# Kernel tuning notes

Measured on AMD Instinct MI355X. Metric: run time of the kernel, lower is better.

Reference implementation:

```python
import jax, jax.numpy as jnp
import numpy as np

N_HEAD = 16
BLOCK_SIZE = 2049  # w2 last dim = block_size - 1 = 2048


def setup_inputs() -> dict:
    key = jax.random.key(0)
    ks = jax.random.split(key, 9)
    B, T, C = 2, 2048, 1024
    hd = C // N_HEAD
    M = BLOCK_SIZE - 1
    return {
        "x": jax.random.normal(ks[0], (B, T, C), jnp.float32),
        "w1_w": jax.random.normal(ks[1], (C, C), jnp.float32) * 0.02,
        "w1_b": jax.random.normal(ks[2], (C,), jnp.float32) * 0.02,
        # torch uniform_(a=-0.001, b=0.001)
        "w2": jax.random.uniform(ks[3], (N_HEAD, hd, M), jnp.float32, -0.001, 0.001),
        "b2": jax.random.normal(ks[4], (M,), jnp.float32) * 0.02,
        "value_w": jax.random.normal(ks[5], (C, C), jnp.float32) * 0.02,
        "value_b": jax.random.normal(ks[6], (C,), jnp.float32) * 0.02,
        "proj_w": jax.random.normal(ks[7], (C, C), jnp.float32) * 0.02,
        "proj_b": jax.random.normal(ks[8], (C,), jnp.float32) * 0.02,
    }


def reference(x, w1_w, w1_b, w2, b2, value_w, value_b, proj_w, proj_b):
    B, T, C = x.shape
    H = N_HEAD
    hd = C // H
    M = w2.shape[-1]  # block_size - 1
    # kernel = relu(w1(x)), split heads -> [B, H, T, hd]
    k = jax.nn.relu(x @ w1_w.T + w1_b).reshape(B, T, H, hd).transpose(0, 2, 1, 3)
    # synthesizer scores: [B, H, T, M]
    attn = jnp.einsum('bhtd,hdm->bhtm', k, w2) + b2
    # causal mask = tril(ones(block,block))[:T, :M] == 0 -> -inf
    causal = jnp.tril(jnp.ones((T, M), dtype=bool))
    attn = jnp.where(causal, attn, -jnp.inf)
    # softmax over first T score columns
    attn = jax.nn.softmax(attn[..., :T], axis=-1)  # [B, H, T, T]
    v = (x @ value_w.T + value_b).reshape(B, T, H, hd).transpose(0, 2, 1, 3)
    out = jnp.einsum('bhts,bhsd->bhtd', attn, v)
    out = out.transpose(0, 2, 1, 3).reshape(B, T, C)
    return out @ proj_w.T + proj_b
```

## Files before the change

kernel.cpp:

```cpp
#include <hip/hip_runtime.h>
#include <math.h>
#include <stdint.h>

typedef __bf16 bf16;
typedef __bf16 bf16x8 __attribute__((ext_vector_type(8)));
typedef __bf16 bf16x4 __attribute__((ext_vector_type(4)));
typedef float f32x4 __attribute__((ext_vector_type(4)));
typedef float f32x16 __attribute__((ext_vector_type(16)));
typedef unsigned int u32;

__device__ __forceinline__ int swz(int row, int chunk) {
    return row * 64 + ((chunk ^ (row & 7)) << 3);
}

__device__ __forceinline__ void gld16(void* lds, const void* g) {
    __builtin_amdgcn_global_load_lds(
        (const __attribute__((address_space(1))) u32*)g,
        (__attribute__((address_space(3))) u32*)lds, 16, 0, 0);
}

__device__ __forceinline__ void stage16(bf16* dst, const bf16* src, size_t srcStride,
                                        int w, int l) {
    #pragma unroll
    for (int i = 0; i < 2; ++i) {
        const int br = w * 16 + i * 8;
        const int r = br + (l >> 3);
        const int gs = (l & 7) ^ (r & 7);
        gld16(dst + br * 64, src + (size_t)r * srcStride + gs * 8);
    }
}

__global__ void cast_bf16_k(const float* __restrict__ src, bf16* __restrict__ dst, int n) {
    const int stride = gridDim.x * blockDim.x * 4;
    for (int i = (blockIdx.x * blockDim.x + threadIdx.x) * 4; i < n; i += stride) {
        float4 v = *(const float4*)(src + i);
        bf16x4 o = {(bf16)v.x, (bf16)v.y, (bf16)v.z, (bf16)v.w};
        *(bf16x4*)(dst + i) = o;
    }
}

__global__ void cast3_bf16_k(const float* __restrict__ s0, bf16* __restrict__ d0,
                             const float* __restrict__ s1, bf16* __restrict__ d1,
                             const float* __restrict__ s2, bf16* __restrict__ d2, int n) {
    const int stride = gridDim.x * blockDim.x * 4;
    for (int i = (blockIdx.x * blockDim.x + threadIdx.x) * 4; i < n; i += stride) {
        float4 v0 = *(const float4*)(s0 + i);
        float4 v1 = *(const float4*)(s1 + i);
        float4 v2 = *(const float4*)(s2 + i);
        bf16x4 o0 = {(bf16)v0.x, (bf16)v0.y, (bf16)v0.z, (bf16)v0.w};
        bf16x4 o1 = {(bf16)v1.x, (bf16)v1.y, (bf16)v1.z, (bf16)v1.w};
        bf16x4 o2 = {(bf16)v2.x, (bf16)v2.y, (bf16)v2.z, (bf16)v2.w};
        *(bf16x4*)(d0 + i) = o0;
        *(bf16x4*)(d1 + i) = o1;
        *(bf16x4*)(d2 + i) = o2;
    }
}

__global__ __launch_bounds__(256) void w2_transpose_k(const float* __restrict__ w2,
                                                      bf16* __restrict__ w2t, int M) {
    __shared__ float Tf[64][65];
    const int h = blockIdx.y, m0 = blockIdx.x * 64, t = threadIdx.x;
    {
        const int dr = t >> 4, c4 = (t & 15) * 4;
        #pragma unroll
        for (int it = 0; it < 4; ++it) {
            const int d = dr + it * 16;
            float4 v = *(const float4*)(w2 + ((size_t)h * 64 + d) * M + m0 + c4);
            Tf[d][c4] = v.x; Tf[d][c4 + 1] = v.y; Tf[d][c4 + 2] = v.z; Tf[d][c4 + 3] = v.w;
        }
    }
    __syncthreads();
    const int m = t >> 2;
    #pragma unroll
    for (int it = 0; it < 2; ++it) {
        const int ch = (t & 3) + it * 4;
        bf16x8 o;
        #pragma unroll
        for (int j = 0; j < 8; ++j) o[j] = (bf16)Tf[ch * 8 + j][m];
        *(bf16x8*)(w2t + ((size_t)h * M + m0 + m) * 64 + ch * 8) = o;
    }
}

__global__ __launch_bounds__(256, 2) void gemm_bf16_k(const bf16* __restrict__ A,
                                                   const bf16* __restrict__ Bw,
                                                   const float* __restrict__ bias,
                                                   const float* __restrict__ bias2,
                                                   float* __restrict__ C0,
                                                   bf16* __restrict__ CK,
                                                   bf16* __restrict__ CV,
                                                   int M, int N, int K, int mode, int Ns)
{
    __shared__ __align__(16) bf16 As[2][128 * 64];
    __shared__ __align__(16) bf16 Bs[2][128 * 64];
    const int tid = threadIdx.x;
    const int w = tid >> 6, l = tid & 63;
    const int wr = w >> 1, wc = w & 1;
    const int lc = l & 15, lg = l >> 4;
    const int row0 = blockIdx.y * 128, col0 = blockIdx.x * 128;

    f32x4 acc[4][4] = {};

    const int nk = K >> 6;
    auto issue = [&](int buf, int k0) {
        #pragma unroll
        for (int i = 0; i < 4; ++i) {
            const int br = (w * 4 + i) * 8;
            const int r = br + (l >> 3);
            const int gs = (l & 7) ^ (r & 7);
            gld16(&As[buf][br * 64], A  + (size_t)(row0 + r) * K + k0 + gs * 8);
            gld16(&Bs[buf][br * 64], Bw + (size_t)(col0 + r) * K + k0 + gs * 8);
        }
    };

    issue(0, 0);
    int cur = 0;
    for (int kt = 0; kt < nk; ++kt) {
        if (kt + 1 < nk) {
            issue(cur ^ 1, (kt + 1) << 6);
            asm volatile("s_waitcnt vmcnt(8)" ::: "memory");
        } else {
            asm volatile("s_waitcnt vmcnt(0)" ::: "memory");
        }
        __builtin_amdgcn_s_barrier();
        #pragma unroll
        for (int ks = 0; ks < 2; ++ks) {
            bf16x8 af[4], bfv[4];
            #pragma unroll
            for (int i = 0; i < 4; ++i) {
                af[i]  = *(const bf16x8*)&As[cur][swz(wr * 64 + i * 16 + lc, ks * 4 + lg)];
                bfv[i] = *(const bf16x8*)&Bs[cur][swz(wc * 64 + i * 16 + lc, ks * 4 + lg)];
            }
            #pragma unroll
            for (int mi = 0; mi < 4; ++mi)
                #pragma unroll
                for (int ni = 0; ni < 4; ++ni)
                    acc[mi][ni] = __builtin_amdgcn_mfma_f32_16x16x32_bf16(af[mi], bfv[ni], acc[mi][ni], 0, 0, 0);
        }
        asm volatile("s_waitcnt lgkmcnt(0)" ::: "memory");
        __builtin_amdgcn_s_barrier();
        cur ^= 1;
    }

    #pragma unroll
    for (int ni = 0; ni < 4; ++ni) {
        const int col = col0 + wc * 64 + ni * 16 + lc;
        #pragma unroll
        for (int mi = 0; mi < 4; ++mi) {
            const int rowb = row0 + wr * 64 + mi * 16 + lg * 4;
            f32x4 v = acc[mi][ni];
            if (mode == 0) {
                const float bv = bias[col];
                #pragma unroll
                for (int r = 0; r < 4; ++r)
                    C0[(size_t)(rowb + r) * N + col] = v[r] + bv;
            } else if (col < Ns) {
                const float bv = bias[col];
                #pragma unroll
                for (int r = 0; r < 4; ++r)
                    CK[(size_t)(rowb + r) * Ns + col] = (bf16)fmaxf(v[r] + bv, 0.f);
            } else {
                const float bv = bias2[col - Ns];
                const int b = rowb >> 11, tt = rowb & 2047;
                bf16x4 o = {(bf16)(v[0] + bv), (bf16)(v[1] + bv),
                            (bf16)(v[2] + bv), (bf16)(v[3] + bv)};
                *(bf16x4*)(CV + ((size_t)b * Ns + (col - Ns)) * 2048 + tt) = o;
            }
        }
    }
}

__global__ __launch_bounds__(256, 2) void synth_attn_v10(const bf16* __restrict__ Kb,
                                                         const bf16* __restrict__ VT,
                                                         const bf16* __restrict__ w2t,
                                                         const float* __restrict__ b2,
                                                         bf16* __restrict__ Ob)
{
    constexpr int T = 2048, C = 1024, M = 2048;
    __shared__ __align__(16) bf16 Wl[3][64 * 64];
    __shared__ __align__(16) bf16 Vl[3][64 * 64];
    __shared__ float b2l[M];
    const int tid = threadIdx.x;
    const int w = tid >> 6, l = tid & 63;
    const int c = l & 31, hi = l >> 5;

    const int bx = blockIdx.x;
    const int hseg = bx >> 8, idx = bx & 255;
    const int jj = idx & 15;
    const int a = hseg ? (15 - jj) : jj;
    const int bh = (hseg << 4) | (idx >> 4);
    const int h = bh & 15, b = bh >> 4;
    const int tA = a, tB = 31 - a;
    const int myT = (w >> 1) ? tA : tB;
    const int t0w = myT * 64 + (w & 1) * 32;

    *(float4*)&b2l[tid * 8]     = *(const float4*)(b2 + tid * 8);
    *(float4*)&b2l[tid * 8 + 4] = *(const float4*)(b2 + tid * 8 + 4);
    __syncthreads();

    const bf16* Wgt = w2t + (size_t)h * M * 64;
    const bf16* Vgt = VT + ((size_t)b * C + h * 64) * T;

    const bf16* Kg = Kb + (size_t)(b * T + t0w + c) * C + h * 64 + hi * 8;
    bf16x8 kf[4];
    #pragma unroll
    for (int kst = 0; kst < 4; ++kst) kf[kst] = *(const bf16x8*)(Kg + kst * 16);

    stage16(&Wl[0][0], Wgt, 64, w, l);
    stage16(&Vl[0][0], Vgt, T, w, l);
    stage16(&Wl[1][0], Wgt + (size_t)64 * 64, 64, w, l);
    stage16(&Vl[1][0], Vgt + 64, T, w, l);

    f32x16 o0 = {}, o1 = {};
    float lsum = 0.f;

    int cur = 0;
    for (int sb = 0; sb <= tB; ++sb) {
        const int s0 = sb * 64;
        if (sb < tB) asm volatile("s_waitcnt vmcnt(4)" ::: "memory");
        else         asm volatile("s_waitcnt vmcnt(0)" ::: "memory");
        __builtin_amdgcn_s_barrier();

        if (sb <= myT) {
            const bf16* Wb = &Wl[cur][0];
            const bf16* Vb = &Vl[cur][0];

            f32x16 sv0, sv1;
            #pragma unroll
            for (int qd = 0; qd < 4; ++qd) {
                float4 b4 = *(const float4*)&b2l[s0 + qd * 8 + 4 * hi];
                float4 b5 = *(const float4*)&b2l[s0 + 32 + qd * 8 + 4 * hi];
                sv0[4*qd] = b4.x; sv0[4*qd+1] = b4.y; sv0[4*qd+2] = b4.z; sv0[4*qd+3] = b4.w;
                sv1[4*qd] = b5.x; sv1[4*qd+1] = b5.y; sv1[4*qd+2] = b5.z; sv1[4*qd+3] = b5.w;
            }
            #pragma unroll
            for (int kst = 0; kst < 4; ++kst) {
                bf16x8 w0 = *(const bf16x8*)&Wb[swz(c,      kst * 2 + hi)];
                bf16x8 w1 = *(const bf16x8*)&Wb[swz(32 + c, kst * 2 + hi)];
                sv0 = __builtin_amdgcn_mfma_f32_32x32x16_bf16(w0, kf[kst], sv0, 0, 0, 0);
                sv1 = __builtin_amdgcn_mfma_f32_32x32x16_bf16(w1, kf[kst], sv1, 0, 0, 0);
            }

            const bool diag = (sb == myT);
            const int qv = (w & 1) * 32 + c;
            u32 U0[8], U1[8];
            #pragma unroll
            for (int qd = 0; qd < 4; ++qd) {
                float e0[4], e1[4];
                #pragma unroll
                for (int k = 0; k < 4; ++k) {
                    const int sbase = qd * 8 + 4 * hi + k;
                    float ev0 = __expf(sv0[4*qd + k]);
                    float ev1 = __expf(sv1[4*qd + k]);
                    if (diag && sbase > qv)      ev0 = 0.f;
                    if (diag && sbase + 32 > qv) ev1 = 0.f;
                    lsum += ev0 + ev1;
                    e0[k] = ev0; e1[k] = ev1;
                }
                union { bf16x4 v; u32 u[2]; } p0, p1;
                p0.v = {(bf16)e0[0], (bf16)e0[1], (bf16)e0[2], (bf16)e0[3]};
                p1.v = {(bf16)e1[0], (bf16)e1[1], (bf16)e1[2], (bf16)e1[3]};
                U0[2*qd] = p0.u[0]; U0[2*qd+1] = p0.u[1];
                U1[2*qd] = p1.u[0]; U1[2*qd+1] = p1.u[1];
            }

            #define PV_TILE(Uarr, st)                                              \
            {                                                                      \
                _Pragma("unroll")                                                  \
                for (int kk = 0; kk < 2; ++kk) {                                   \
                    u32 A00 = Uarr[4*kk],   A01 = Uarr[4*kk+1];                    \
                    u32 A10 = Uarr[4*kk+2], A11 = Uarr[4*kk+3];                    \
                    u32 s00 = (u32)__shfl_xor((int)A00, 32);                       \
                    u32 s01 = (u32)__shfl_xor((int)A01, 32);                       \
                    u32 s10 = (u32)__shfl_xor((int)A10, 32);                       \
                    u32 s11 = (u32)__shfl_xor((int)A11, 32);                       \
                    union { u32 u[4]; bf16x8 v; } pa;                              \
                    pa.u[0] = hi ? s10 : A00;                                      \
                    pa.u[1] = hi ? s11 : A01;                                      \
                    pa.u[2] = hi ? A10 : s00;                                      \
                    pa.u[3] = hi ? A11 : s01;                                      \
                    const int ch = (st) * 4 + kk * 2 + hi;                         \
                    bf16x8 v0 = *(const bf16x8*)&Vb[swz(c,      ch)];              \
                    bf16x8 v1 = *(const bf16x8*)&Vb[swz(32 + c, ch)];              \
                    o0 = __builtin_amdgcn_mfma_f32_32x32x16_bf16(pa.v, v0, o0, 0, 0, 0); \
                    o1 = __builtin_amdgcn_mfma_f32_32x32x16_bf16(pa.v, v1, o1, 0, 0, 0); \
                }                                                                  \
            }
            PV_TILE(U0, 0)
            PV_TILE(U1, 1)
            #undef PV_TILE
        }

        if (sb + 2 <= tB) {
            int nx = cur + 2; if (nx >= 3) nx -= 3;
            stage16(&Wl[nx][0], Wgt + (size_t)(s0 + 128) * 64, 64, w, l);
            stage16(&Vl[nx][0], Vgt + (s0 + 128), T, w, l);
        }
        if (++cur == 3) cur = 0;
    }

    const float inv = 1.f / (lsum + __shfl_xor(lsum, 32));
    #pragma unroll
    for (int r = 0; r < 16; ++r) {
        const int q_ = (r & 3) + 8 * (r >> 2) + 4 * hi;
        const float iv = __shfl(inv, q_);
        bf16* dst = Ob + (size_t)(b * T + t0w + q_) * C + h * 64;
        dst[c]      = (bf16)(o0[r] * iv);
        dst[32 + c] = (bf16)(o1[r] * iv);
    }
}

extern "C" void kernel_launch(void* const* d_in, const int* in_sizes, int n_in,
                              void* d_out, int out_size, void* d_ws, size_t ws_size,
                              hipStream_t stream) {
    const float* x       = (const float*)d_in[0];
    const float* w1_w    = (const float*)d_in[1];
    const float* w1_b    = (const float*)d_in[2];
    const float* w2      = (const float*)d_in[3];
    const float* b2      = (const float*)d_in[4];
    const float* value_w = (const float*)d_in[5];
    const float* value_b = (const float*)d_in[6];
    const float* proj_w  = (const float*)d_in[7];
    const float* proj_b  = (const float*)d_in[8];

    const int B = 2, T = 2048, C = 1024, H = 16, M = 2048;
    const int R = B * T;

    bf16* xb  = (bf16*)d_ws;
    bf16* w1b = xb  + (size_t)R * C;
    bf16* vwb = w1b + (size_t)C * C;
    bf16* w2t = vwb + (size_t)C * C;
    bf16* pwb = w2t + (size_t)H * M * 64;
    bf16* Kb  = pwb + (size_t)C * C;
    bf16* VTb = Kb  + (size_t)R * C;
    bf16* Ob  = VTb + (size_t)R * C;

    cast_bf16_k<<<1024, 256, 0, stream>>>(x, xb, R * C);
    cast3_bf16_k<<<512, 256, 0, stream>>>(w1_w, w1b, value_w, vwb, proj_w, pwb, C * C);
    w2_transpose_k<<<dim3(M / 64, H), 256, 0, stream>>>(w2, w2t, M);

    gemm_bf16_k<<<dim3(2 * C / 128, R / 128), 256, 0, stream>>>(
        xb, w1b, w1_b, value_b, nullptr, Kb, VTb, R, 2 * C, C, 1, C);

    synth_attn_v10<<<dim3(512), 256, 0, stream>>>(Kb, VTb, w2t, b2, Ob);

    gemm_bf16_k<<<dim3(C / 128, R / 128), 256, 0, stream>>>(
        Ob, pwb, proj_b, nullptr, (float*)d_out, nullptr, nullptr, R, C, C, 0, C);
}
```

Baseline: 113.7 us.

## Split attention KV range across two wave groups with LDS reduction

```diff
diff --git a/kernel.cpp b/kernel.cpp
--- a/kernel.cpp
+++ b/kernel.cpp
@@ -17,17 +17,6 @@
     __builtin_amdgcn_global_load_lds(
         (const __attribute__((address_space(1))) u32*)g,
         (__attribute__((address_space(3))) u32*)lds, 16, 0, 0);
-}
-
-__device__ __forceinline__ void stage16(bf16* dst, const bf16* src, size_t srcStride,
-                                        int w, int l) {
-    #pragma unroll
-    for (int i = 0; i < 2; ++i) {
-        const int br = w * 16 + i * 8;
-        const int r = br + (l >> 3);
-        const int gs = (l & 7) ^ (r & 7);
-        gld16(dst + br * 64, src + (size_t)r * srcStride + gs * 8);
-    }
 }
 
 __global__ void cast_bf16_k(const float* __restrict__ src, bf16* __restrict__ dst, int n) {
@@ -169,60 +158,80 @@
     }
 }
 
-__global__ __launch_bounds__(256, 2) void synth_attn_v10(const bf16* __restrict__ Kb,
+__global__ __launch_bounds__(512, 4) void synth_attn_v11(const bf16* __restrict__ Kb,
                                                          const bf16* __restrict__ VT,
                                                          const bf16* __restrict__ w2t,
                                                          const float* __restrict__ b2,
                                                          bf16* __restrict__ Ob)
 {
     constexpr int T = 2048, C = 1024, M = 2048;
-    __shared__ __align__(16) bf16 Wl[3][64 * 64];
-    __shared__ __align__(16) bf16 Vl[3][64 * 64];
+    __shared__ __align__(16) bf16 ring[2][2][8192];
     __shared__ float b2l[M];
     const int tid = threadIdx.x;
     const int w = tid >> 6, l = tid & 63;
     const int c = l & 31, hi = l >> 5;
+    const int sg = w & 1, qh = w >> 1;
 
     const int bx = blockIdx.x;
-    const int hseg = bx >> 8, idx = bx & 255;
-    const int jj = idx & 15;
-    const int a = hseg ? (15 - jj) : jj;
-    const int bh = (hseg << 4) | (idx >> 4);
+    const int u = bx & 255, rg = bx >> 8;
+    const int t128 = rg ? (15 - (u & 15)) : (u & 15);
+    const int bh = (u >> 4) + (rg << 4);
     const int h = bh & 15, b = bh >> 4;
-    const int tA = a, tB = 31 - a;
-    const int myT = (w >> 1) ? tA : tB;
-    const int t0w = myT * 64 + (w & 1) * 32;
-
-    *(float4*)&b2l[tid * 8]     = *(const float4*)(b2 + tid * 8);
-    *(float4*)&b2l[tid * 8 + 4] = *(const float4*)(b2 + tid * 8 + 4);
+    const int t0w = t128 * 128 + qh * 32;
+    const int myT = 2 * t128 + (qh >> 1);
+
+    *(float4*)&b2l[tid * 4] = *(const float4*)(b2 + tid * 4);
     __syncthreads();
 
-    const bf16* Wgt = w2t + (size_t)h * M * 64;
-    const bf16* Vgt = VT + ((size_t)b * C + h * 64) * T;
-
-    const bf16* Kg = Kb + (size_t)(b * T + t0w + c) * C + h * 64 + hi * 8;
+    const bf16* Wg = w2t + (size_t)h * M * 64;
+    const bf16* Vg = VT + ((size_t)b * C + h * 64) * T;
+
+    const bf16* Kg = Kb + ((size_t)(b * T + t0w + c)) * C + h * 64 + hi * 8;
     bf16x8 kf[4];
     #pragma unroll
     for (int kst = 0; kst < 4; ++kst) kf[kst] = *(const bf16x8*)(Kg + kst * 16);
 
-    stage16(&Wl[0][0], Wgt, 64, w, l);
-    stage16(&Vl[0][0], Vgt, T, w, l);
-    stage16(&Wl[1][0], Wgt + (size_t)64 * 64, 64, w, l);
-    stage16(&Vl[1][0], Vgt + 64, T, w, l);
+    auto stage = [&](int buf, int sb) {
+        bf16* dst = &ring[sg][buf][0];
+        const int s0 = sb * 64;
+        const int jb = (qh & 1) * 4;
+        if (qh < 2) {
+            #pragma unroll
+            for (int j = 0; j < 4; ++j) {
+                const int jj = jb + j, r = jj >> 2, kst = jj & 3;
+                gld16(dst + jj * 512,
+                      Wg + ((size_t)(s0 + r * 32 + c)) * 64 + kst * 16 + hi * 8);
+            }
+        } else {
+            #pragma unroll
+            for (int j = 0; j < 4; ++j) {
+                const int jj = jb + j, r = jj >> 2, m = jj & 3;
+                gld16(dst + 4096 + jj * 512,
+                      Vg + ((size_t)(r * 32 + c)) * T + s0 + m * 16 + hi * 8);
+            }
+        }
+    };
+
+    const int nIter = t128 + 1;
+    stage(0, sg);
 
     f32x16 o0 = {}, o1 = {};
     float lsum = 0.f;
 
-    int cur = 0;
-    for (int sb = 0; sb <= tB; ++sb) {
-        const int s0 = sb * 64;
-        if (sb < tB) asm volatile("s_waitcnt vmcnt(4)" ::: "memory");
-        else         asm volatile("s_waitcnt vmcnt(0)" ::: "memory");
+    for (int i = 0; i < nIter; ++i) {
+        const int sb = 2 * i + sg;
+        if (i + 1 < nIter) {
+            stage((i + 1) & 1, sb + 2);
+            asm volatile("s_waitcnt vmcnt(4)" ::: "memory");
+        } else {
+            asm volatile("s_waitcnt vmcnt(0)" ::: "memory");
+        }
         __builtin_amdgcn_s_barrier();
 
         if (sb <= myT) {
-            const bf16* Wb = &Wl[cur][0];
-            const bf16* Vb = &Vl[cur][0];
+            const bf16* Wb = &ring[sg][i & 1][0];
+            const bf16* Vb = &ring[sg][i & 1][4096];
+            const int s0 = sb * 64;
 
             f32x16 sv0, sv1;
             #pragma unroll
@@ -234,14 +243,14 @@
             }
             #pragma unroll
             for (int kst = 0; kst < 4; ++kst) {
-                bf16x8 w0 = *(const bf16x8*)&Wb[swz(c,      kst * 2 + hi)];
-                bf16x8 w1 = *(const bf16x8*)&Wb[swz(32 + c, kst * 2 + hi)];
+                bf16x8 w0 = *(const bf16x8*)&Wb[kst * 512 + l * 8];
+                bf16x8 w1 = *(const bf16x8*)&Wb[(4 + kst) * 512 + l * 8];
                 sv0 = __builtin_amdgcn_mfma_f32_32x32x16_bf16(w0, kf[kst], sv0, 0, 0, 0);
                 sv1 = __builtin_amdgcn_mfma_f32_32x32x16_bf16(w1, kf[kst], sv1, 0, 0, 0);
             }
 
             const bool diag = (sb == myT);
-            const int qv = (w & 1) * 32 + c;
+            const int qv = (qh & 1) * 32 + c;
             u32 U0[8], U1[8];
             #pragma unroll
             for (int qd = 0; qd < 4; ++qd) {
@@ -256,11 +265,11 @@
                     lsum += ev0 + ev1;
                     e0[k] = ev0; e1[k] = ev1;
                 }
-                union { bf16x4 v; u32 u[2]; } p0, p1;
+                union { bf16x4 v; u32 uu[2]; } p0, p1;
                 p0.v = {(bf16)e0[0], (bf16)e0[1], (bf16)e0[2], (bf16)e0[3]};
                 p1.v = {(bf16)e1[0], (bf16)e1[1], (bf16)e1[2], (bf16)e1[3]};
-                U0[2*qd] = p0.u[0]; U0[2*qd+1] = p0.u[1];
-                U1[2*qd] = p1.u[0]; U1[2*qd+1] = p1.u[1];
+                U0[2*qd] = p0.uu[0]; U0[2*qd+1] = p0.uu[1];
+                U1[2*qd] = p1.uu[0]; U1[2*qd+1] = p1.uu[1];
             }
 
             #define PV_TILE(Uarr, st)                                              \
@@ -273,14 +282,14 @@
                     u32 s01 = (u32)__shfl_xor((int)A01, 32);                       \
                     u32 s10 = (u32)__shfl_xor((int)A10, 32);                       \
                     u32 s11 = (u32)__shfl_xor((int)A11, 32);                       \
-                    union { u32 u[4]; bf16x8 v; } pa;                              \
-                    pa.u[0] = hi ? s10 : A00;                                      \
-                    pa.u[1] = hi ? s11 : A01;                                      \
-                    pa.u[2] = hi ? A10 : s00;                                      \
-                    pa.u[3] = hi ? A11 : s01;                                      \
-                    const int ch = (st) * 4 + kk * 2 + hi;                         \
-                    bf16x8 v0 = *(const bf16x8*)&Vb[swz(c,      ch)];              \
-                    bf16x8 v1 = *(const bf16x8*)&Vb[swz(32 + c, ch)];              \
+                    union { u32 uu[4]; bf16x8 v; } pa;                             \
+                    pa.uu[0] = hi ? s10 : A00;                                     \
+                    pa.uu[1] = hi ? s11 : A01;                                     \
+                    pa.uu[2] = hi ? A10 : s00;                                     \
+                    pa.uu[3] = hi ? A11 : s01;                                     \
+                    const int m = (st) * 2 + kk;                                   \
+                    bf16x8 v0 = *(const bf16x8*)&Vb[m * 512 + l * 8];              \
+                    bf16x8 v1 = *(const bf16x8*)&Vb[(4 + m) * 512 + l * 8];        \
                     o0 = __builtin_amdgcn_mfma_f32_32x32x16_bf16(pa.v, v0, o0, 0, 0, 0); \
                     o1 = __builtin_amdgcn_mfma_f32_32x32x16_bf16(pa.v, v1, o1, 0, 0, 0); \
                 }                                                                  \
@@ -290,22 +299,35 @@
             #undef PV_TILE
         }
 
-        if (sb + 2 <= tB) {
-            int nx = cur + 2; if (nx >= 3) nx -= 3;
-            stage16(&Wl[nx][0], Wgt + (size_t)(s0 + 128) * 64, 64, w, l);
-            stage16(&Vl[nx][0], Vgt + (s0 + 128), T, w, l);
-        }
-        if (++cur == 3) cur = 0;
-    }
-
-    const float inv = 1.f / (lsum + __shfl_xor(lsum, 32));
-    #pragma unroll
-    for (int r = 0; r < 16; ++r) {
-        const int q_ = (r & 3) + 8 * (r >> 2) + 4 * hi;
-        const float iv = __shfl(inv, q_);
-        bf16* dst = Ob + (size_t)(b * T + t0w + q_) * C + h * 64;
-        dst[c]      = (bf16)(o0[r] * iv);
-        dst[32 + c] = (bf16)(o1[r] * iv);
+        asm volatile("s_waitcnt lgkmcnt(0)" ::: "memory");
+        __builtin_amdgcn_s_barrier();
+    }
+
+    float* scr = (float*)&ring[0][0][0];
+    float* base = scr + qh * 2112;
+    if (sg == 1) {
+        #pragma unroll
+        for (int k = 0; k < 16; ++k) base[k * 64 + l] = o0[k];
+        #pragma unroll
+        for (int k = 0; k < 16; ++k) base[(16 + k) * 64 + l] = o1[k];
+        base[32 * 64 + l] = lsum;
+    }
+    __syncthreads();
+    if (sg == 0) {
+        #pragma unroll
+        for (int k = 0; k < 16; ++k) o0[k] += base[k * 64 + l];
+        #pragma unroll
+        for (int k = 0; k < 16; ++k) o1[k] += base[(16 + k) * 64 + l];
+        lsum += base[32 * 64 + l];
+        const float inv = 1.f / (lsum + __shfl_xor(lsum, 32));
+        #pragma unroll
+        for (int r = 0; r < 16; ++r) {
+            const int q_ = (r & 3) + 8 * (r >> 2) + 4 * hi;
+            const float iv = __shfl(inv, q_);
+            bf16* dst = Ob + (size_t)(b * T + t0w + q_) * C + h * 64;
+            dst[c]      = (bf16)(o0[r] * iv);
+            dst[32 + c] = (bf16)(o1[r] * iv);
+        }
     }
 }
 
@@ -341,7 +363,7 @@
     gemm_bf16_k<<<dim3(2 * C / 128, R / 128), 256, 0, stream>>>(
         xb, w1b, w1_b, value_b, nullptr, Kb, VTb, R, 2 * C, C, 1, C);
 
-    synth_attn_v10<<<dim3(512), 256, 0, stream>>>(Kb, VTb, w2t, b2, Ob);
+    synth_attn_v11<<<dim3(512), 512, 0, stream>>>(Kb, VTb, w2t, b2, Ob);
 
     gemm_bf16_k<<<dim3(C / 128, R / 128), 256, 0, stream>>>(
         Ob, pwb, proj_b, nullptr, (float*)d_out, nullptr, nullptr, R, C, C, 0, C);
```

New measurement: 109.9 us. -3.3%, faster.
